# Performance work log

Hardware: AMD Instinct MI355X
Metric: run time of the kernel (lower is better)

## Reference

```python
import jax, jax.numpy as jnp
import numpy as np

CROSS_NUM, EXPERT_NUM, LOW_RANK = 3, 4, 64
BATCH, DIM = 32768, 512


def setup_inputs() -> dict:
    key = jax.random.key(0)
    ks = jax.random.split(key, 6)
    s = 0.05  # small init so tanh stays in its linear-ish range
    return {
        "x": jax.random.normal(ks[0], (BATCH, DIM), dtype=jnp.float32),
        "Vs": jax.random.normal(ks[1], (CROSS_NUM, EXPERT_NUM, LOW_RANK, DIM), dtype=jnp.float32) * s,
        "Cs": jax.random.normal(ks[2], (CROSS_NUM, EXPERT_NUM, LOW_RANK, LOW_RANK), dtype=jnp.float32) * s,
        "Us": jax.random.normal(ks[3], (CROSS_NUM, EXPERT_NUM, DIM, LOW_RANK), dtype=jnp.float32) * s,
        "bias": jax.random.normal(ks[4], (CROSS_NUM, DIM), dtype=jnp.float32) * s,
        "gate_w": jax.random.normal(ks[5], (DIM, EXPERT_NUM), dtype=jnp.float32) * s,
    }


def reference(x, Vs, Cs, Us, bias, gate_w):
    # x: [B, D]. The original keeps a trailing singleton axis; we drop it and
    # batch the per-expert einsum chain over the expert axis e.
    x0 = x
    x_l = x
    for i in range(CROSS_NUM):
        # gating (shared Dense(1) per expert, applied to current x_l): [B, E]
        g = x_l @ gate_w
        # low-rank expert chain, batched over experts
        v = jnp.tanh(jnp.einsum('eld,bd->bel', Vs[i], x_l))   # [B, E, low]
        c = jnp.tanh(jnp.einsum('elk,bek->bel', Cs[i], v))    # [B, E, low]
        u = jnp.einsum('edl,bel->bed', Us[i], c)              # [B, E, D]
        expert_out = (u + bias[i][None, None, :]) * x0[:, None, :]  # [B, E, D]
        # mixture combine (raw gating scores, no softmax, as in original)
        moe = jnp.einsum('bed,be->bd', expert_out, g)
        x_l = moe + x_l
    return x_l
```

## Files before the change

### kernel.cpp

```cpp
#include <hip/hip_runtime.h>
#include <hip/hip_bf16.h>


#define CROSS   3
#define ENUM    4
#define LR      64
#define ELD     256
#define DIM     512
#define BATCH   32768
#define BT      64
#define NTHR    1024

#define XL_W    520
#define Y_W     264

typedef __bf16 bf16x8 __attribute__((ext_vector_type(8)));
typedef float  f32x4  __attribute__((ext_vector_type(4)));
typedef unsigned short us;
typedef unsigned short us4 __attribute__((ext_vector_type(4)));

__device__ __forceinline__ us f2bf(float f) {
    return __builtin_bit_cast(us, (__bf16)f);
}
__device__ __forceinline__ float bf2f(us b) {
    unsigned int u = ((unsigned int)b) << 16;
    return __builtin_bit_cast(float, u);
}
__device__ __forceinline__ float tanh_fast(float x) {
    float t = __expf(2.f * x);
    return (t - 1.f) * __builtin_amdgcn_rcpf(t + 1.f);
}

#define MFMA(a, b, c) __builtin_amdgcn_mfma_f32_16x16x32_bf16(a, b, c, 0, 0, 0)

__device__ __forceinline__ void gload_lds16(const us* g, us* l) {
    __builtin_amdgcn_global_load_lds(
        (const __attribute__((address_space(1))) unsigned int*)g,
        (__attribute__((address_space(3))) unsigned int*)l, 16, 0, 0);
}

#define WAITN(n)  asm volatile("s_waitcnt vmcnt(" #n ")" ::: "memory")
#define SBAR0()   __builtin_amdgcn_sched_barrier(0)
#define LBAR() do { SBAR0(); \
    asm volatile("s_waitcnt lgkmcnt(0)" ::: "memory"); \
    __builtin_amdgcn_s_barrier(); SBAR0(); } while (0)

__global__ __launch_bounds__(64) void swz_all(
    const float* __restrict__ Vs, const float* __restrict__ Cs,
    const float* __restrict__ Us,
    us* __restrict__ Vf, us* __restrict__ Cf, us* __restrict__ Uf)
{
    int b = blockIdx.x;
    int lane = threadIdx.x;
    const float* src;
    us* dst;
    if (b < 768) {
        int i = b >> 8, t = b & 255;
        int nt = t >> 4, ks = t & 15;
        int n  = nt * 16 + (lane & 15);
        int k0 = ks * 32 + (lane >> 4) * 8;
        src = Vs + (size_t)i * ELD * DIM + (size_t)n * DIM + k0;
        dst = Vf + (size_t)i * ELD * DIM
            + ((size_t)(nt * 16 + ks) * 64 + lane) * 8;
    } else if (b < 1536) {
        int bb = b - 768;
        int i = bb >> 8, t = bb & 255;
        int nt = t >> 3, ks = t & 7;
        int n  = nt * 16 + (lane & 15);
        int k0 = ks * 32 + (lane >> 4) * 8;
        int e = k0 >> 6, l0 = k0 & 63;
        src = Us + (size_t)i * ENUM * DIM * LR
            + (size_t)e * DIM * LR + (size_t)n * LR + l0;
        dst = Uf + (size_t)i * DIM * ELD
            + ((size_t)(nt * 8 + ks) * 64 + lane) * 8;
    } else {
        int bb = b - 1536;
        int i = bb >> 5, rest = bb & 31;
        int e = rest >> 3, t = rest & 7;
        int nt = t >> 1, ks = t & 1;
        int n  = nt * 16 + (lane & 15);
        int k0 = ks * 32 + (lane >> 4) * 8;
        src = Cs + (((size_t)(i * ENUM + e) * LR + n) * LR) + k0;
        dst = Cf + (size_t)i * ENUM * LR * LR
            + ((size_t)((e * 4 + nt) * 2 + ks) * 64 + lane) * 8;
    }
    f32x4 s0 = *reinterpret_cast<const f32x4*>(src);
    f32x4 s1 = *reinterpret_cast<const f32x4*>(src + 4);
    us4 p0, p1;
    p0[0] = f2bf(s0[0]); p0[1] = f2bf(s0[1]); p0[2] = f2bf(s0[2]); p0[3] = f2bf(s0[3]);
    p1[0] = f2bf(s1[0]); p1[1] = f2bf(s1[1]); p1[2] = f2bf(s1[2]); p1[3] = f2bf(s1[3]);
    *reinterpret_cast<us4*>(dst)     = p0;
    *reinterpret_cast<us4*>(dst + 4) = p1;
}

__global__ __launch_bounds__(NTHR, 4) void dcn_fused(
    const float* __restrict__ x,
    float* __restrict__ out,
    const us* __restrict__ Vf,
    const us* __restrict__ Cf,
    const us* __restrict__ Uf,
    const float* __restrict__ gw,
    const float* __restrict__ bias)
{
    __shared__ us xl_s[BT * XL_W];
    __shared__ us y_s[BT * Y_W];
    __shared__ us ring_s[16 * 3 * 512];
    __shared__ us gw_s[4 * 512];
    __shared__ __align__(16) float g_s[BT * ENUM];
    __shared__ __align__(16) float sc[NTHR];

    const int tid  = threadIdx.x;
    const int wave = tid >> 6, lane = tid & 63;
    const int quad = lane >> 4, nl = lane & 15;
    const int rh = wave >> 3, wc = wave & 7;
    const int rh32 = rh * 32;
    const int row0 = blockIdx.x * BT;
    us* wring = &ring_s[wave * 1536];

#define ISSUE_V(f) gload_lds16( \
    Vl + ((size_t)((wc * 2 + ((f) & 1)) * 16 + ((f) >> 1)) * 64 + lane) * 8, \
    wring + ((f) % 3) * 512)
#define ISSUE_U(f) gload_lds16( \
    Ul + ((size_t)((wc * 4 + ((f) & 3)) * 8 + ((f) >> 2)) * 64 + lane) * 8, \
    wring + ((f) % 3) * 512)

    #pragma unroll
    for (int it = 0; it < 8; ++it) {
        int f4 = tid + it * NTHR;
        int r = f4 >> 7, c4 = f4 & 127;
        f32x4 v = __builtin_nontemporal_load(
            reinterpret_cast<const f32x4*>(
                x + (size_t)(row0 + r) * DIM + c4 * 4));
        us4 p;
        p[0] = f2bf(v[0]); p[1] = f2bf(v[1]); p[2] = f2bf(v[2]); p[3] = f2bf(v[3]);
        *reinterpret_cast<us4*>(&xl_s[r * XL_W + c4 * 4]) = p;
    }
    #pragma unroll
    for (int j = 0; j < 2; ++j) {
        int idx = tid * 2 + j;
        int e = idx >> 9, d = idx & 511;
        gw_s[idx] = f2bf(gw[(size_t)d * ENUM + e]);
    }
    LBAR();

    unsigned int x0p[2][4][2];
    #pragma unroll
    for (int mt = 0; mt < 2; ++mt)
        #pragma unroll
        for (int nt = 0; nt < 4; ++nt) {
            int rb = rh32 + mt * 16 + quad * 4;
            int col = wc * 64 + nt * 16 + nl;
            unsigned int b0 = xl_s[(rb + 0) * XL_W + col];
            unsigned int b1 = xl_s[(rb + 1) * XL_W + col];
            unsigned int b2 = xl_s[(rb + 2) * XL_W + col];
            unsigned int b3 = xl_s[(rb + 3) * XL_W + col];
            x0p[mt][nt][0] = b0 | (b1 << 16);
            x0p[mt][nt][1] = b2 | (b3 << 16);
        }

    const int e = wc >> 1, h = wc & 1;

    #pragma unroll 1
    for (int layer = 0; layer < CROSS; ++layer) {
        const us* Vl = Vf + (size_t)layer * ELD * DIM;
        const us* Cl = Cf + (size_t)layer * ENUM * LR * LR;
        const us* Ul = Uf + (size_t)layer * DIM * ELD;
        const float* bl = bias + layer * DIM;

        ISSUE_V(0); ISSUE_V(1);
        LBAR();

        {
            int grow = tid >> 4, ge = (tid >> 2) & 3, gq = tid & 3;
            float gp = 0.f;
            #pragma unroll
            for (int dd = 0; dd < 16; ++dd) {
                int d0 = gq * 128 + ((dd + gq * 4) & 15) * 8;
                bf16x8 xa = *reinterpret_cast<const bf16x8*>(
                    &xl_s[grow * XL_W + d0]);
                bf16x8 wa = *reinterpret_cast<const bf16x8*>(
                    &gw_s[ge * 512 + d0]);
                #pragma unroll
                for (int j = 0; j < 8; ++j)
                    gp += (float)xa[j] * (float)wa[j];
            }
            sc[tid] = gp;
        }
        LBAR();
        if (tid < 256)
            g_s[tid] = sc[tid * 4] + sc[tid * 4 + 1]
                     + sc[tid * 4 + 2] + sc[tid * 4 + 3];

        f32x4 acc1[2][2];
        acc1[0][0] = (f32x4)0.f; acc1[0][1] = (f32x4)0.f;
        acc1[1][0] = (f32x4)0.f; acc1[1][1] = (f32x4)0.f;
        #pragma unroll
        for (int ks = 0; ks < 16; ++ks) {
            bf16x8 a0 = *reinterpret_cast<const bf16x8*>(
                &xl_s[(rh32 + nl) * XL_W + ks * 32 + quad * 8]);
            bf16x8 a1 = *reinterpret_cast<const bf16x8*>(
                &xl_s[(rh32 + 16 + nl) * XL_W + ks * 32 + quad * 8]);
            #pragma unroll
            for (int nt = 0; nt < 2; ++nt) {
                const int f = ks * 2 + nt;
                if (f < 31) { WAITN(1); } else { WAITN(0); }
                SBAR0();
                bf16x8 b = *reinterpret_cast<const bf16x8*>(
                    &wring[(f % 3) * 512 + lane * 8]);
                acc1[0][nt] = MFMA(a0, b, acc1[0][nt]);
                acc1[1][nt] = MFMA(a1, b, acc1[1][nt]);
                SBAR0();
                if (f + 2 < 32) { ISSUE_V(f + 2); }
            }
        }
        bf16x8 creg[2][2];
        #pragma unroll
        for (int ks = 0; ks < 2; ++ks)
            #pragma unroll
            for (int nt = 0; nt < 2; ++nt)
                creg[ks][nt] = *reinterpret_cast<const bf16x8*>(
                    &Cl[((size_t)((e * 4 + h * 2 + nt) * 2 + ks) * 64 + lane) * 8]);
        float bias_r[4];
        #pragma unroll
        for (int nt = 0; nt < 4; ++nt)
            bias_r[nt] = bl[wc * 64 + nt * 16 + nl];
        ISSUE_U(0); ISSUE_U(1);

        #pragma unroll
        for (int mt = 0; mt < 2; ++mt)
            #pragma unroll
            for (int r = 0; r < 4; ++r) {
                int row = rh32 + mt * 16 + quad * 4 + r;
                #pragma unroll
                for (int nt = 0; nt < 2; ++nt)
                    y_s[row * Y_W + wc * 32 + nt * 16 + nl] =
                        f2bf(tanh_fast(acc1[mt][nt][r]));
            }
        LBAR();

        float Gv[2][4];
        #pragma unroll
        for (int mt = 0; mt < 2; ++mt)
            #pragma unroll
            for (int r = 0; r < 4; ++r) {
                int row = rh32 + mt * 16 + quad * 4 + r;
                f32x4 g4 = *reinterpret_cast<const f32x4*>(&g_s[row * ENUM]);
                Gv[mt][r] = g4[0] + g4[1] + g4[2] + g4[3];
            }

        f32x4 acc2[2][2];
        acc2[0][0] = (f32x4)0.f; acc2[0][1] = (f32x4)0.f;
        acc2[1][0] = (f32x4)0.f; acc2[1][1] = (f32x4)0.f;
        #pragma unroll
        for (int ks = 0; ks < 2; ++ks) {
            bf16x8 a0 = *reinterpret_cast<const bf16x8*>(
                &y_s[(rh32 + nl) * Y_W + e * 64 + ks * 32 + quad * 8]);
            bf16x8 a1 = *reinterpret_cast<const bf16x8*>(
                &y_s[(rh32 + 16 + nl) * Y_W + e * 64 + ks * 32 + quad * 8]);
            #pragma unroll
            for (int nt = 0; nt < 2; ++nt) {
                acc2[0][nt] = MFMA(a0, creg[ks][nt], acc2[0][nt]);
                acc2[1][nt] = MFMA(a1, creg[ks][nt], acc2[1][nt]);
            }
        }
        LBAR();
        #pragma unroll
        for (int mt = 0; mt < 2; ++mt)
            #pragma unroll
            for (int r = 0; r < 4; ++r) {
                int row = rh32 + mt * 16 + quad * 4 + r;
                float gv = g_s[row * ENUM + e];
                #pragma unroll
                for (int nt = 0; nt < 2; ++nt)
                    y_s[row * Y_W + e * 64 + h * 32 + nt * 16 + nl] =
                        f2bf(tanh_fast(acc2[mt][nt][r]) * gv);
            }
        LBAR();

        f32x4 acc3[2][4];
        #pragma unroll
        for (int mt = 0; mt < 2; ++mt)
            #pragma unroll
            for (int nt = 0; nt < 4; ++nt) acc3[mt][nt] = (f32x4)0.f;
        #pragma unroll
        for (int ks = 0; ks < 8; ++ks) {
            bf16x8 a0 = *reinterpret_cast<const bf16x8*>(
                &y_s[(rh32 + nl) * Y_W + ks * 32 + quad * 8]);
            bf16x8 a1 = *reinterpret_cast<const bf16x8*>(
                &y_s[(rh32 + 16 + nl) * Y_W + ks * 32 + quad * 8]);
            #pragma unroll
            for (int nt = 0; nt < 4; ++nt) {
                const int f = ks * 4 + nt;
                if (f < 31) { WAITN(1); } else { WAITN(0); }
                SBAR0();
                bf16x8 b = *reinterpret_cast<const bf16x8*>(
                    &wring[(f % 3) * 512 + lane * 8]);
                acc3[0][nt] = MFMA(a0, b, acc3[0][nt]);
                acc3[1][nt] = MFMA(a1, b, acc3[1][nt]);
                SBAR0();
                if (f + 2 < 32) { ISSUE_U(f + 2); }
            }
        }

        #pragma unroll
        for (int nt = 0; nt < 4; ++nt) {
            int col = wc * 64 + nt * 16 + nl;
            #pragma unroll
            for (int mt = 0; mt < 2; ++mt)
                #pragma unroll
                for (int r = 0; r < 4; ++r) {
                    int row = rh32 + mt * 16 + quad * 4 + r;
                    float x0v = bf2f(
                        (us)(x0p[mt][nt][r >> 1] >> ((r & 1) * 16)));
                    float xlo = bf2f(xl_s[row * XL_W + col]);
                    float res = xlo
                              + x0v * (acc3[mt][nt][r] + bias_r[nt] * Gv[mt][r]);
                    if (layer == CROSS - 1)
                        __builtin_nontemporal_store(
                            res, &out[(size_t)(row0 + row) * DIM + col]);
                    else
                        xl_s[row * XL_W + col] = f2bf(res);
                }
        }
    }
#undef ISSUE_V
#undef ISSUE_U
}

extern "C" void kernel_launch(void* const* d_in, const int* in_sizes, int n_in,
                              void* d_out, int out_size, void* d_ws,
                              size_t ws_size, hipStream_t stream) {
    const float* x      = (const float*)d_in[0];
    const float* Vs     = (const float*)d_in[1];
    const float* Cs     = (const float*)d_in[2];
    const float* Us     = (const float*)d_in[3];
    const float* bias   = (const float*)d_in[4];
    const float* gate_w = (const float*)d_in[5];
    float* out = (float*)d_out;

    us* Vf = (us*)d_ws;
    us* Uf = Vf + (size_t)CROSS * ELD * DIM;
    us* Cf = Uf + (size_t)CROSS * DIM * ELD;

    swz_all<<<1632, 64, 0, stream>>>(Vs, Cs, Us, Vf, Cf, Uf);
    dcn_fused<<<BATCH / BT, NTHR, 0, stream>>>(x, out, Vf, Cf, Uf,
                                               gate_w, bias);
}
```

Baseline: 325.3 us.

## Share weight staging across waves with block-wide triple-buffered LDS pipeline

Replaces the per-wave private weight ring with a block-shared triple-buffered staging area. Each wave now loads a distinct slice of V/U, so the two row-halves no longer both fetch the same weights, halving global weight traffic per block. The cost is a full block barrier per pipeline step instead of wave-local syncs. The change also hoists the C/bias loads to the top of each layer, reuses y_s as the gating reduction scratch, and switches the final output store from nontemporal to a normal store.

```diff
diff --git a/kernel.cpp b/kernel.cpp
--- a/kernel.cpp
+++ b/kernel.cpp
@@ -103,11 +103,11 @@
     const float* __restrict__ bias)
 {
     __shared__ us xl_s[BT * XL_W];
-    __shared__ us y_s[BT * Y_W];
-    __shared__ us ring_s[16 * 3 * 512];
+    __shared__ __align__(16) us y_s[BT * Y_W];
+    __shared__ us stg_s[3 * 8192];
     __shared__ us gw_s[4 * 512];
     __shared__ __align__(16) float g_s[BT * ENUM];
-    __shared__ __align__(16) float sc[NTHR];
+    float* sc = reinterpret_cast<float*>(y_s);
 
     const int tid  = threadIdx.x;
     const int wave = tid >> 6, lane = tid & 63;
@@ -115,14 +115,14 @@
     const int rh = wave >> 3, wc = wave & 7;
     const int rh32 = rh * 32;
     const int row0 = blockIdx.x * BT;
-    us* wring = &ring_s[wave * 1536];
-
-#define ISSUE_V(f) gload_lds16( \
-    Vl + ((size_t)((wc * 2 + ((f) & 1)) * 16 + ((f) >> 1)) * 64 + lane) * 8, \
-    wring + ((f) % 3) * 512)
-#define ISSUE_U(f) gload_lds16( \
-    Ul + ((size_t)((wc * 4 + ((f) & 3)) * 8 + ((f) >> 2)) * 64 + lane) * 8, \
-    wring + ((f) % 3) * 512)
+
+#define ISSUE_V(k) gload_lds16( \
+    Vl + ((size_t)(wave * 16 + (k)) * 64 + lane) * 8, \
+    stg_s + ((k) % 3) * 8192 + wave * 512)
+#define ISSUE_U(s) gload_lds16( \
+    Ul + ((size_t)(((wave >> 1) * 4 + ((s) & 1) * 2 + (wave & 1)) * 8 \
+                   + ((s) >> 1)) * 64 + lane) * 8, \
+    stg_s + ((s) % 3) * 8192 + wave * 512)
 
     #pragma unroll
     for (int it = 0; it < 8; ++it) {
@@ -167,6 +167,18 @@
         const us* Ul = Uf + (size_t)layer * DIM * ELD;
         const float* bl = bias + layer * DIM;
 
+        bf16x8 creg[2][2];
+        #pragma unroll
+        for (int ks = 0; ks < 2; ++ks)
+            #pragma unroll
+            for (int nt = 0; nt < 2; ++nt)
+                creg[ks][nt] = *reinterpret_cast<const bf16x8*>(
+                    &Cl[((size_t)((e * 4 + h * 2 + nt) * 2 + ks) * 64 + lane) * 8]);
+        float bias_r[4];
+        #pragma unroll
+        for (int nt = 0; nt < 4; ++nt)
+            bias_r[nt] = bl[wc * 64 + nt * 16 + nl];
+
         ISSUE_V(0); ISSUE_V(1);
         LBAR();
 
@@ -196,36 +208,22 @@
         acc1[1][0] = (f32x4)0.f; acc1[1][1] = (f32x4)0.f;
         #pragma unroll
         for (int ks = 0; ks < 16; ++ks) {
+            if (ks < 15) { WAITN(1); } else { WAITN(0); }
+            LBAR();
+            if (ks + 2 < 16) { ISSUE_V(ks + 2); }
             bf16x8 a0 = *reinterpret_cast<const bf16x8*>(
                 &xl_s[(rh32 + nl) * XL_W + ks * 32 + quad * 8]);
             bf16x8 a1 = *reinterpret_cast<const bf16x8*>(
                 &xl_s[(rh32 + 16 + nl) * XL_W + ks * 32 + quad * 8]);
+            const us* sl = stg_s + (ks % 3) * 8192;
             #pragma unroll
             for (int nt = 0; nt < 2; ++nt) {
-                const int f = ks * 2 + nt;
-                if (f < 31) { WAITN(1); } else { WAITN(0); }
-                SBAR0();
                 bf16x8 b = *reinterpret_cast<const bf16x8*>(
-                    &wring[(f % 3) * 512 + lane * 8]);
+                    &sl[(wc * 2 + nt) * 512 + lane * 8]);
                 acc1[0][nt] = MFMA(a0, b, acc1[0][nt]);
                 acc1[1][nt] = MFMA(a1, b, acc1[1][nt]);
-                SBAR0();
-                if (f + 2 < 32) { ISSUE_V(f + 2); }
-            }
-        }
-        bf16x8 creg[2][2];
-        #pragma unroll
-        for (int ks = 0; ks < 2; ++ks)
-            #pragma unroll
-            for (int nt = 0; nt < 2; ++nt)
-                creg[ks][nt] = *reinterpret_cast<const bf16x8*>(
-                    &Cl[((size_t)((e * 4 + h * 2 + nt) * 2 + ks) * 64 + lane) * 8]);
-        float bias_r[4];
-        #pragma unroll
-        for (int nt = 0; nt < 4; ++nt)
-            bias_r[nt] = bl[wc * 64 + nt * 16 + nl];
-        ISSUE_U(0); ISSUE_U(1);
-
+            }
+        }
         #pragma unroll
         for (int mt = 0; mt < 2; ++mt)
             #pragma unroll
@@ -236,6 +234,7 @@
                     y_s[row * Y_W + wc * 32 + nt * 16 + nl] =
                         f2bf(tanh_fast(acc1[mt][nt][r]));
             }
+        ISSUE_U(0); ISSUE_U(1);
         LBAR();
 
         float Gv[2][4];
@@ -275,30 +274,33 @@
                     y_s[row * Y_W + e * 64 + h * 32 + nt * 16 + nl] =
                         f2bf(tanh_fast(acc2[mt][nt][r]) * gv);
             }
-        LBAR();
 
         f32x4 acc3[2][4];
         #pragma unroll
         for (int mt = 0; mt < 2; ++mt)
             #pragma unroll
             for (int nt = 0; nt < 4; ++nt) acc3[mt][nt] = (f32x4)0.f;
-        #pragma unroll
-        for (int ks = 0; ks < 8; ++ks) {
-            bf16x8 a0 = *reinterpret_cast<const bf16x8*>(
-                &y_s[(rh32 + nl) * Y_W + ks * 32 + quad * 8]);
-            bf16x8 a1 = *reinterpret_cast<const bf16x8*>(
-                &y_s[(rh32 + 16 + nl) * Y_W + ks * 32 + quad * 8]);
-            #pragma unroll
-            for (int nt = 0; nt < 4; ++nt) {
-                const int f = ks * 4 + nt;
-                if (f < 31) { WAITN(1); } else { WAITN(0); }
-                SBAR0();
+        bf16x8 za0, za1;
+        #pragma unroll
+        for (int s = 0; s < 16; ++s) {
+            if (s < 15) { WAITN(1); } else { WAITN(0); }
+            LBAR();
+            if (s + 2 < 16) { ISSUE_U(s + 2); }
+            if ((s & 1) == 0) {
+                int ks = s >> 1;
+                za0 = *reinterpret_cast<const bf16x8*>(
+                    &y_s[(rh32 + nl) * Y_W + ks * 32 + quad * 8]);
+                za1 = *reinterpret_cast<const bf16x8*>(
+                    &y_s[(rh32 + 16 + nl) * Y_W + ks * 32 + quad * 8]);
+            }
+            const us* sl = stg_s + (s % 3) * 8192;
+            const int nb = (s & 1) * 2;
+            #pragma unroll
+            for (int j = 0; j < 2; ++j) {
                 bf16x8 b = *reinterpret_cast<const bf16x8*>(
-                    &wring[(f % 3) * 512 + lane * 8]);
-                acc3[0][nt] = MFMA(a0, b, acc3[0][nt]);
-                acc3[1][nt] = MFMA(a1, b, acc3[1][nt]);
-                SBAR0();
-                if (f + 2 < 32) { ISSUE_U(f + 2); }
+                    &sl[(wc * 2 + j) * 512 + lane * 8]);
+                acc3[0][nb + j] = MFMA(za0, b, acc3[0][nb + j]);
+                acc3[1][nb + j] = MFMA(za1, b, acc3[1][nb + j]);
             }
         }
 
@@ -316,8 +318,7 @@
                     float res = xlo
                               + x0v * (acc3[mt][nt][r] + bias_r[nt] * Gv[mt][r]);
                     if (layer == CROSS - 1)
-                        __builtin_nontemporal_store(
-                            res, &out[(size_t)(row0 + row) * DIM + col]);
+                        out[(size_t)(row0 + row) * DIM + col] = res;
                     else
                         xl_s[row * XL_W + col] = f2bf(res);
                 }
```

New measurement: 322.0 us. About the same (-1.0%).

## Halve block tile to 32 rows with 512 threads and deepen weight prefetch ring

Applied to the files above, without the earlier changes.

Shrinks the per-block batch tile from 64 to 32 rows and the block from 1024 to 512 threads, so each wave owns all rows and one 64-column slice. It also aliases the gating scratch onto y_s and cuts the ring buffer to lower LDS use and allow more resident blocks. The weight prefetch now keeps three slots in flight instead of two. C-weight loads are hoisted ahead of the V GEMM, and the U prefetch is issued after the tanh store. The running x_l is kept in registers so the epilogue skips an LDS read, and nontemporal load/store hints are dropped. The trade-off is that each block streams the V/U weights for half as many rows, doubling weight traffic per row.

```diff
diff --git a/kernel.cpp b/kernel.cpp
--- a/kernel.cpp
+++ b/kernel.cpp
@@ -8,8 +8,8 @@
 #define ELD     256
 #define DIM     512
 #define BATCH   32768
-#define BT      64
-#define NTHR    1024
+#define BT      32
+#define NTHR    512
 
 #define XL_W    520
 #define Y_W     264
@@ -25,6 +25,9 @@
 __device__ __forceinline__ float bf2f(us b) {
     unsigned int u = ((unsigned int)b) << 16;
     return __builtin_bit_cast(float, u);
+}
+__device__ __forceinline__ unsigned int pack2(float lo, float hi) {
+    return (unsigned int)f2bf(lo) | ((unsigned int)f2bf(hi) << 16);
 }
 __device__ __forceinline__ float tanh_fast(float x) {
     float t = __expf(2.f * x);
@@ -44,6 +47,12 @@
 #define LBAR() do { SBAR0(); \
     asm volatile("s_waitcnt lgkmcnt(0)" ::: "memory"); \
     __builtin_amdgcn_s_barrier(); SBAR0(); } while (0)
+
+__device__ __forceinline__ void wait_slot(int left) {
+    if (left >= 2)      WAITN(2);
+    else if (left == 1) WAITN(1);
+    else                WAITN(0);
+}
 
 __global__ __launch_bounds__(64) void swz_all(
     const float* __restrict__ Vs, const float* __restrict__ Cs,
@@ -103,17 +112,16 @@
     const float* __restrict__ bias)
 {
     __shared__ us xl_s[BT * XL_W];
-    __shared__ us y_s[BT * Y_W];
-    __shared__ us ring_s[16 * 3 * 512];
+    __shared__ __align__(16) us y_s[BT * Y_W];
+    __shared__ us ring_s[8 * 1536];
     __shared__ us gw_s[4 * 512];
     __shared__ __align__(16) float g_s[BT * ENUM];
-    __shared__ __align__(16) float sc[NTHR];
+    float* sc = reinterpret_cast<float*>(y_s);
 
     const int tid  = threadIdx.x;
     const int wave = tid >> 6, lane = tid & 63;
     const int quad = lane >> 4, nl = lane & 15;
-    const int rh = wave >> 3, wc = wave & 7;
-    const int rh32 = rh * 32;
+    const int wc   = wave;
     const int row0 = blockIdx.x * BT;
     us* wring = &ring_s[wave * 1536];
 
@@ -128,27 +136,27 @@
     for (int it = 0; it < 8; ++it) {
         int f4 = tid + it * NTHR;
         int r = f4 >> 7, c4 = f4 & 127;
-        f32x4 v = __builtin_nontemporal_load(
-            reinterpret_cast<const f32x4*>(
-                x + (size_t)(row0 + r) * DIM + c4 * 4));
+        f32x4 v = *reinterpret_cast<const f32x4*>(
+            x + (size_t)(row0 + r) * DIM + c4 * 4);
         us4 p;
         p[0] = f2bf(v[0]); p[1] = f2bf(v[1]); p[2] = f2bf(v[2]); p[3] = f2bf(v[3]);
         *reinterpret_cast<us4*>(&xl_s[r * XL_W + c4 * 4]) = p;
     }
     #pragma unroll
-    for (int j = 0; j < 2; ++j) {
-        int idx = tid * 2 + j;
+    for (int j = 0; j < 4; ++j) {
+        int idx = tid * 4 + j;
         int e = idx >> 9, d = idx & 511;
         gw_s[idx] = f2bf(gw[(size_t)d * ENUM + e]);
     }
     LBAR();
 
     unsigned int x0p[2][4][2];
+    unsigned int xlr[2][4][2];
     #pragma unroll
     for (int mt = 0; mt < 2; ++mt)
         #pragma unroll
         for (int nt = 0; nt < 4; ++nt) {
-            int rb = rh32 + mt * 16 + quad * 4;
+            int rb = mt * 16 + quad * 4;
             int col = wc * 64 + nt * 16 + nl;
             unsigned int b0 = xl_s[(rb + 0) * XL_W + col];
             unsigned int b1 = xl_s[(rb + 1) * XL_W + col];
@@ -156,6 +164,8 @@
             unsigned int b3 = xl_s[(rb + 3) * XL_W + col];
             x0p[mt][nt][0] = b0 | (b1 << 16);
             x0p[mt][nt][1] = b2 | (b3 << 16);
+            xlr[mt][nt][0] = x0p[mt][nt][0];
+            xlr[mt][nt][1] = x0p[mt][nt][1];
         }
 
     const int e = wc >> 1, h = wc & 1;
@@ -167,7 +177,14 @@
         const us* Ul = Uf + (size_t)layer * DIM * ELD;
         const float* bl = bias + layer * DIM;
 
-        ISSUE_V(0); ISSUE_V(1);
+        bf16x8 creg[2][2];
+        #pragma unroll
+        for (int ks = 0; ks < 2; ++ks)
+            #pragma unroll
+            for (int nt = 0; nt < 2; ++nt)
+                creg[ks][nt] = *reinterpret_cast<const bf16x8*>(
+                    &Cl[((size_t)((e * 4 + h * 2 + nt) * 2 + ks) * 64 + lane) * 8]);
+        ISSUE_V(0); ISSUE_V(1); ISSUE_V(2);
         LBAR();
 
         {
@@ -187,7 +204,7 @@
             sc[tid] = gp;
         }
         LBAR();
-        if (tid < 256)
+        if (tid < 128)
             g_s[tid] = sc[tid * 4] + sc[tid * 4 + 1]
                      + sc[tid * 4 + 2] + sc[tid * 4 + 3];
 
@@ -197,45 +214,33 @@
         #pragma unroll
         for (int ks = 0; ks < 16; ++ks) {
             bf16x8 a0 = *reinterpret_cast<const bf16x8*>(
-                &xl_s[(rh32 + nl) * XL_W + ks * 32 + quad * 8]);
+                &xl_s[(nl) * XL_W + ks * 32 + quad * 8]);
             bf16x8 a1 = *reinterpret_cast<const bf16x8*>(
-                &xl_s[(rh32 + 16 + nl) * XL_W + ks * 32 + quad * 8]);
+                &xl_s[(16 + nl) * XL_W + ks * 32 + quad * 8]);
             #pragma unroll
             for (int nt = 0; nt < 2; ++nt) {
                 const int f = ks * 2 + nt;
-                if (f < 31) { WAITN(1); } else { WAITN(0); }
+                wait_slot(31 - f);
                 SBAR0();
                 bf16x8 b = *reinterpret_cast<const bf16x8*>(
                     &wring[(f % 3) * 512 + lane * 8]);
                 acc1[0][nt] = MFMA(a0, b, acc1[0][nt]);
                 acc1[1][nt] = MFMA(a1, b, acc1[1][nt]);
                 SBAR0();
-                if (f + 2 < 32) { ISSUE_V(f + 2); }
-            }
-        }
-        bf16x8 creg[2][2];
-        #pragma unroll
-        for (int ks = 0; ks < 2; ++ks)
-            #pragma unroll
-            for (int nt = 0; nt < 2; ++nt)
-                creg[ks][nt] = *reinterpret_cast<const bf16x8*>(
-                    &Cl[((size_t)((e * 4 + h * 2 + nt) * 2 + ks) * 64 + lane) * 8]);
-        float bias_r[4];
-        #pragma unroll
-        for (int nt = 0; nt < 4; ++nt)
-            bias_r[nt] = bl[wc * 64 + nt * 16 + nl];
-        ISSUE_U(0); ISSUE_U(1);
-
+                if (f + 3 < 32) { ISSUE_V(f + 3); }
+            }
+        }
         #pragma unroll
         for (int mt = 0; mt < 2; ++mt)
             #pragma unroll
             for (int r = 0; r < 4; ++r) {
-                int row = rh32 + mt * 16 + quad * 4 + r;
+                int row = mt * 16 + quad * 4 + r;
                 #pragma unroll
                 for (int nt = 0; nt < 2; ++nt)
                     y_s[row * Y_W + wc * 32 + nt * 16 + nl] =
                         f2bf(tanh_fast(acc1[mt][nt][r]));
             }
+        ISSUE_U(0); ISSUE_U(1); ISSUE_U(2);
         LBAR();
 
         float Gv[2][4];
@@ -243,7 +248,7 @@
         for (int mt = 0; mt < 2; ++mt)
             #pragma unroll
             for (int r = 0; r < 4; ++r) {
-                int row = rh32 + mt * 16 + quad * 4 + r;
+                int row = mt * 16 + quad * 4 + r;
                 f32x4 g4 = *reinterpret_cast<const f32x4*>(&g_s[row * ENUM]);
                 Gv[mt][r] = g4[0] + g4[1] + g4[2] + g4[3];
             }
@@ -254,9 +259,9 @@
         #pragma unroll
         for (int ks = 0; ks < 2; ++ks) {
             bf16x8 a0 = *reinterpret_cast<const bf16x8*>(
-                &y_s[(rh32 + nl) * Y_W + e * 64 + ks * 32 + quad * 8]);
+                &y_s[(nl) * Y_W + e * 64 + ks * 32 + quad * 8]);
             bf16x8 a1 = *reinterpret_cast<const bf16x8*>(
-                &y_s[(rh32 + 16 + nl) * Y_W + e * 64 + ks * 32 + quad * 8]);
+                &y_s[(16 + nl) * Y_W + e * 64 + ks * 32 + quad * 8]);
             #pragma unroll
             for (int nt = 0; nt < 2; ++nt) {
                 acc2[0][nt] = MFMA(a0, creg[ks][nt], acc2[0][nt]);
@@ -268,7 +273,7 @@
         for (int mt = 0; mt < 2; ++mt)
             #pragma unroll
             for (int r = 0; r < 4; ++r) {
-                int row = rh32 + mt * 16 + quad * 4 + r;
+                int row = mt * 16 + quad * 4 + r;
                 float gv = g_s[row * ENUM + e];
                 #pragma unroll
                 for (int nt = 0; nt < 2; ++nt)
@@ -285,42 +290,53 @@
         #pragma unroll
         for (int ks = 0; ks < 8; ++ks) {
             bf16x8 a0 = *reinterpret_cast<const bf16x8*>(
-                &y_s[(rh32 + nl) * Y_W + ks * 32 + quad * 8]);
+                &y_s[(nl) * Y_W + ks * 32 + quad * 8]);
             bf16x8 a1 = *reinterpret_cast<const bf16x8*>(
-                &y_s[(rh32 + 16 + nl) * Y_W + ks * 32 + quad * 8]);
+                &y_s[(16 + nl) * Y_W + ks * 32 + quad * 8]);
             #pragma unroll
             for (int nt = 0; nt < 4; ++nt) {
                 const int f = ks * 4 + nt;
-                if (f < 31) { WAITN(1); } else { WAITN(0); }
+                wait_slot(31 - f);
                 SBAR0();
                 bf16x8 b = *reinterpret_cast<const bf16x8*>(
                     &wring[(f % 3) * 512 + lane * 8]);
                 acc3[0][nt] = MFMA(a0, b, acc3[0][nt]);
                 acc3[1][nt] = MFMA(a1, b, acc3[1][nt]);
                 SBAR0();
-                if (f + 2 < 32) { ISSUE_U(f + 2); }
-            }
-        }
+                if (f + 3 < 32) { ISSUE_U(f + 3); }
+            }
+        }
+
+        float bias_r[4];
+        #pragma unroll
+        for (int nt = 0; nt < 4; ++nt)
+            bias_r[nt] = bl[wc * 64 + nt * 16 + nl];
 
         #pragma unroll
         for (int nt = 0; nt < 4; ++nt) {
             int col = wc * 64 + nt * 16 + nl;
             #pragma unroll
-            for (int mt = 0; mt < 2; ++mt)
+            for (int mt = 0; mt < 2; ++mt) {
+                float res[4];
                 #pragma unroll
                 for (int r = 0; r < 4; ++r) {
-                    int row = rh32 + mt * 16 + quad * 4 + r;
+                    int row = mt * 16 + quad * 4 + r;
                     float x0v = bf2f(
                         (us)(x0p[mt][nt][r >> 1] >> ((r & 1) * 16)));
-                    float xlo = bf2f(xl_s[row * XL_W + col]);
-                    float res = xlo
-                              + x0v * (acc3[mt][nt][r] + bias_r[nt] * Gv[mt][r]);
+                    float xlo = bf2f(
+                        (us)(xlr[mt][nt][r >> 1] >> ((r & 1) * 16)));
+                    res[r] = xlo
+                           + x0v * (acc3[mt][nt][r] + bias_r[nt] * Gv[mt][r]);
                     if (layer == CROSS - 1)
-                        __builtin_nontemporal_store(
-                            res, &out[(size_t)(row0 + row) * DIM + col]);
+                        out[(size_t)(row0 + row) * DIM + col] = res[r];
                     else
-                        xl_s[row * XL_W + col] = f2bf(res);
+                        xl_s[row * XL_W + col] = f2bf(res[r]);
                 }
+                if (layer < CROSS - 1) {
+                    xlr[mt][nt][0] = pack2(res[0], res[1]);
+                    xlr[mt][nt][1] = pack2(res[2], res[3]);
+                }
+            }
         }
     }
 #undef ISSUE_V
```

Measured after the change: 390.4 us. 1.2x slower.
